# Kernel tuning notes

Measured on AMD Instinct MI355X. Metric: run time of the kernel, lower is better.

Reference implementation:

```python
import jax, jax.numpy as jnp
import numpy as np

N_HEAD = 16

def setup_inputs() -> dict:
    key = jax.random.key(0)
    ks = jax.random.split(key, 8)
    B, S, D = 2, 2048, 1024
    s = 0.02
    return {
        "x": jax.random.normal(ks[0], (B, S, D), dtype=jnp.float32),
        "Wq": jax.random.normal(ks[1], (D, D), dtype=jnp.float32) * s,
        "bq": jax.random.normal(ks[2], (D,), dtype=jnp.float32) * s,
        "Wk": jax.random.normal(ks[3], (D, D), dtype=jnp.float32) * s,
        "Wv": jax.random.normal(ks[4], (D, D), dtype=jnp.float32) * s,
        "bv": jax.random.normal(ks[5], (D,), dtype=jnp.float32) * s,
        "Wo": jax.random.normal(ks[6], (D, D), dtype=jnp.float32) * s,
        "bo": jax.random.normal(ks[7], (D,), dtype=jnp.float32) * s,
    }

def reference(x, Wq, bq, Wk, Wv, bv, Wo, bo):
    B, S, D = x.shape
    H = N_HEAD
    dh = D // H
    scale = dh ** -0.25
    # projections (torch F.linear: x @ W.T + b)
    q = x @ Wq.T + bq
    k = x @ Wk.T              # key has no bias
    v = x @ Wv.T + bv
    # split heads: [B, H, S, dh]
    q = q.reshape(B, S, H, dh).transpose(0, 2, 1, 3) * scale
    k = k.reshape(B, S, H, dh).transpose(0, 2, 1, 3) * scale
    v = v.reshape(B, S, H, dh).transpose(0, 2, 1, 3)
    qk = jnp.einsum('bhqd,bhkd->bhqk', q, k)
    w = jax.nn.softmax(qk.astype(jnp.float32), axis=-1).astype(q.dtype)
    wv = jnp.einsum('bhqk,bhkd->bhqd', w, v)
    wv = wv.transpose(0, 2, 1, 3).reshape(B, S, D)
    out = wv @ Wo.T + bo
    return out, w
```

## Files before the change

### kernel.cpp

```cpp
#include <hip/hip_runtime.h>

typedef float  f32x4 __attribute__((ext_vector_type(4)));
typedef short  s16x8 __attribute__((ext_vector_type(8)));
typedef unsigned short u16x4 __attribute__((ext_vector_type(4)));


static __device__ __forceinline__ unsigned short f2bf(float f) {
  unsigned u = __builtin_bit_cast(unsigned, f);
  u += 0x7fffu + ((u >> 16) & 1u);
  return (unsigned short)(u >> 16);
}

static __device__ __forceinline__ void glds16(const void* g, void* l) {
  __builtin_amdgcn_global_load_lds(
      (const __attribute__((address_space(1))) unsigned int*)g,
      (__attribute__((address_space(3))) unsigned int*)l, 16, 0, 0);
}

__global__ __launch_bounds__(256) void cvt_bf16(const float4* __restrict__ src,
                                                u16x4* __restrict__ dst) {
  int i = blockIdx.x * 256 + threadIdx.x;
  float4 v = src[i];
  u16x4 o = { f2bf(v.x), f2bf(v.y), f2bf(v.z), f2bf(v.w) };
  dst[i] = o;
}

__global__ __launch_bounds__(256) void gemm_nt(const unsigned short* __restrict__ A,
                                               const unsigned short* __restrict__ Bm,
                                               const float* __restrict__ bias,
                                               float scale, int mode,
                                               void* __restrict__ out) {
  __shared__ unsigned short at[128 * 64];
  __shared__ unsigned short bt[128 * 64];
  const int tid = threadIdx.x, lane = tid & 63, wid = tid >> 6;
  const int l15 = lane & 15, l4 = lane >> 4;
  const int nb = (blockIdx.x & 7) * 128, mb = (blockIdx.x >> 3) * 128;
  const int wm = (wid >> 1) * 64, wn = (wid & 1) * 64;

  f32x4 acc[4][4];
#pragma unroll
  for (int mt = 0; mt < 4; ++mt)
#pragma unroll
    for (int nt = 0; nt < 4; ++nt) acc[mt][nt] = {0.f, 0.f, 0.f, 0.f};

  for (int k0 = 0; k0 < 1024; k0 += 64) {
#pragma unroll
    for (int i = 0; i < 4; ++i) {
      int slotbase = (i * 4 + wid) * 64;
      int slot = slotbase + lane;
      int row = slot >> 3;
      int cs = (slot & 7) ^ (row & 7);
      glds16(&A[(mb + row) * 1024 + k0 + cs * 8], &at[slotbase * 8]);
      glds16(&Bm[(nb + row) * 1024 + k0 + cs * 8], &bt[slotbase * 8]);
    }
    __syncthreads();
#pragma unroll
    for (int ks = 0; ks < 2; ++ks) {
      s16x8 af[4], bf[4];
#pragma unroll
      for (int mt = 0; mt < 4; ++mt) {
        int row = wm + mt * 16 + l15;
        af[mt] = *(const s16x8*)((const char*)&at[row * 64] +
                                 ((ks * 64 + l4 * 16) ^ ((row & 7) << 4)));
      }
#pragma unroll
      for (int nt = 0; nt < 4; ++nt) {
        int row = wn + nt * 16 + l15;
        bf[nt] = *(const s16x8*)((const char*)&bt[row * 64] +
                                 ((ks * 64 + l4 * 16) ^ ((row & 7) << 4)));
      }
#pragma unroll
      for (int mt = 0; mt < 4; ++mt)
#pragma unroll
        for (int nt = 0; nt < 4; ++nt)
          acc[mt][nt] = __builtin_amdgcn_mfma_f32_16x16x32_bf16(af[mt], bf[nt],
                                                                acc[mt][nt], 0, 0, 0);
    }
    __syncthreads();
  }

#pragma unroll
  for (int mt = 0; mt < 4; ++mt)
#pragma unroll
    for (int nt = 0; nt < 4; ++nt) {
      int n = nb + wn + nt * 16 + l15;
      float bvv = bias ? bias[n] : 0.0f;
      int m0 = mb + wm + mt * 16 + l4 * 4;
      if (mode == 0) {
#pragma unroll
        for (int r = 0; r < 4; ++r) {
          int m = m0 + r;
          float v = (acc[mt][nt][r] + bvv) * scale;
          int bb = m >> 11, s = m & 2047, hh = n >> 6, d = n & 63;
          ((unsigned short*)out)[(size_t)((bb * 16 + hh) * 2048 + s) * 64 + d] = f2bf(v);
        }
      } else if (mode == 1) {
        int bb = m0 >> 11, s0 = m0 & 2047, hh = n >> 6, d = n & 63;
        u16x4 p;
#pragma unroll
        for (int r = 0; r < 4; ++r) p[r] = f2bf(acc[mt][nt][r] + bvv);
        *(u16x4*)&((unsigned short*)out)[(size_t)((bb * 16 + hh) * 64 + d) * 2048 + s0] = p;
      } else {
#pragma unroll
        for (int r = 0; r < 4; ++r) {
          int m = m0 + r;
          ((float*)out)[(size_t)m * 1024 + n] = acc[mt][nt][r] + bvv;
        }
      }
    }
}

__global__ __launch_bounds__(256) void attn_sumexp(const unsigned short* __restrict__ Q,
                                                   const unsigned short* __restrict__ K,
                                                   float* __restrict__ lsum) {
  __shared__ unsigned short kt[64 * 64];
  const int tid = threadIdx.x, lane = tid & 63, wid = tid >> 6;
  const int l15 = lane & 15, l4 = lane >> 4;
  const int bh = blockIdx.x >> 5;
  const int qb = (blockIdx.x & 31) * 64;
  const int q = qb + wid * 16 + l15;

  s16x8 qf[2];
  qf[0] = *(const s16x8*)&Q[(bh * 2048 + q) * 64 + l4 * 8];
  qf[1] = *(const s16x8*)&Q[(bh * 2048 + q) * 64 + 32 + l4 * 8];

  float acc = 0.f;
  for (int k0 = 0; k0 < 2048; k0 += 64) {
#pragma unroll
    for (int i = 0; i < 2; ++i) {
      int slotbase = (i * 4 + wid) * 64;
      int slot = slotbase + lane;
      int row = slot >> 3;
      int cs = (slot & 7) ^ (row & 7);
      glds16(&K[(bh * 2048 + k0 + row) * 64 + cs * 8], &kt[slotbase * 8]);
    }
    __syncthreads();
#pragma unroll
    for (int ks = 0; ks < 4; ++ks) {
      f32x4 c = {0.f, 0.f, 0.f, 0.f};
      int row = ks * 16 + l15;
#pragma unroll
      for (int t = 0; t < 2; ++t) {
        s16x8 a = *(const s16x8*)((const char*)&kt[row * 64] +
                                  ((t * 64 + l4 * 16) ^ ((row & 7) << 4)));
        c = __builtin_amdgcn_mfma_f32_16x16x32_bf16(a, qf[t], c, 0, 0, 0);
      }
      acc += __expf(c[0]) + __expf(c[1]) + __expf(c[2]) + __expf(c[3]);
    }
    __syncthreads();
  }
  acc += __shfl_xor(acc, 16);
  acc += __shfl_xor(acc, 32);
  if (l4 == 0) lsum[bh * 2048 + q] = acc;
}

__global__ __launch_bounds__(256) void attn_wv(const unsigned short* __restrict__ Q,
                                               const unsigned short* __restrict__ K,
                                               const unsigned short* __restrict__ Vt,
                                               const float* __restrict__ lsum,
                                               float* __restrict__ wout,
                                               unsigned short* __restrict__ wv) {
  __shared__ unsigned short kt[64 * 64];
  __shared__ unsigned short vt[64 * 64];
  __shared__ unsigned short pt[4][16 * 64];
  const int tid = threadIdx.x, lane = tid & 63, wid = tid >> 6;
  const int l15 = lane & 15, l4 = lane >> 4;
  const int bh = blockIdx.x >> 5;
  const int qb = (blockIdx.x & 31) * 64;
  const int q = qb + wid * 16 + l15;

  s16x8 qf[2];
  qf[0] = *(const s16x8*)&Q[(bh * 2048 + q) * 64 + l4 * 8];
  qf[1] = *(const s16x8*)&Q[(bh * 2048 + q) * 64 + 32 + l4 * 8];
  float rcpl = 1.0f / lsum[bh * 2048 + q];
  float* wrow = &wout[((size_t)bh * 2048 + q) * 2048];

  f32x4 oacc[4];
#pragma unroll
  for (int dt = 0; dt < 4; ++dt) oacc[dt] = {0.f, 0.f, 0.f, 0.f};

  for (int k0i = 0; k0i < 32; ++k0i) {
    int k0 = k0i * 64;
#pragma unroll
    for (int i = 0; i < 2; ++i) {
      int slotbase = (i * 4 + wid) * 64;
      int slot = slotbase + lane;
      int row = slot >> 3;
      int cs = (slot & 7) ^ (row & 7);
      glds16(&K[(bh * 2048 + k0 + row) * 64 + cs * 8], &kt[slotbase * 8]);
      glds16(&Vt[(size_t)(bh * 64 + row) * 2048 + k0 + cs * 8], &vt[slotbase * 8]);
    }
    __syncthreads();
#pragma unroll
    for (int ks = 0; ks < 4; ++ks) {
      f32x4 c = {0.f, 0.f, 0.f, 0.f};
      int row = ks * 16 + l15;
#pragma unroll
      for (int t = 0; t < 2; ++t) {
        s16x8 a = *(const s16x8*)((const char*)&kt[row * 64] +
                                  ((t * 64 + l4 * 16) ^ ((row & 7) << 4)));
        c = __builtin_amdgcn_mfma_f32_16x16x32_bf16(a, qf[t], c, 0, 0, 0);
      }
      float w0 = __expf(c[0]) * rcpl, w1 = __expf(c[1]) * rcpl;
      float w2 = __expf(c[2]) * rcpl, w3 = __expf(c[3]) * rcpl;
      f32x4 w4 = {w0, w1, w2, w3};
      *(f32x4*)&wrow[k0 + ks * 16 + l4 * 4] = w4;
      u16x4 pb = {f2bf(w0), f2bf(w1), f2bf(w2), f2bf(w3)};
      *(u16x4*)((char*)&pt[wid][l15 * 64] +
                ((ks * 32 + l4 * 8) ^ ((l15 & 7) << 4))) = pb;
    }
#pragma unroll
    for (int t = 0; t < 2; ++t) {
      s16x8 pa = *(const s16x8*)((const char*)&pt[wid][l15 * 64] +
                                 ((t * 64 + l4 * 16) ^ ((l15 & 7) << 4)));
#pragma unroll
      for (int dt = 0; dt < 4; ++dt) {
        int row = dt * 16 + l15;
        s16x8 vb = *(const s16x8*)((const char*)&vt[row * 64] +
                                   ((t * 64 + l4 * 16) ^ ((row & 7) << 4)));
        oacc[dt] = __builtin_amdgcn_mfma_f32_16x16x32_bf16(pa, vb, oacc[dt], 0, 0, 0);
      }
    }
    __syncthreads();
  }
  int b = bh >> 4, h = bh & 15;
#pragma unroll
  for (int dt = 0; dt < 4; ++dt)
#pragma unroll
    for (int r = 0; r < 4; ++r) {
      int sq = qb + wid * 16 + l4 * 4 + r;
      int d = dt * 16 + l15;
      wv[(size_t)(b * 2048 + sq) * 1024 + h * 64 + d] = f2bf(oacc[dt][r]);
    }
}

extern "C" void kernel_launch(void* const* d_in, const int* in_sizes, int n_in,
                              void* d_out, int out_size, void* d_ws, size_t ws_size,
                              hipStream_t stream) {
  const float* x  = (const float*)d_in[0];
  const float* Wq = (const float*)d_in[1];
  const float* bq = (const float*)d_in[2];
  const float* Wk = (const float*)d_in[3];
  const float* Wv = (const float*)d_in[4];
  const float* bv = (const float*)d_in[5];
  const float* bo = (const float*)d_in[7];
  const float* Wo = (const float*)d_in[6];
  float* out  = (float*)d_out;
  float* wout = out + 4194304;

  unsigned short* xb  = (unsigned short*)d_ws;
  unsigned short* Wqb = xb + 4194304;
  unsigned short* Wkb = Wqb + 1048576;
  unsigned short* Wvb = Wkb + 1048576;
  unsigned short* Wob = Wvb + 1048576;
  unsigned short* Qb  = Wob + 1048576;
  unsigned short* Kb  = Qb + 4194304;
  unsigned short* Vtb = Kb + 4194304;
  float* lsum = (float*)(Vtb + 4194304);
  unsigned short* wvb = xb;

  cvt_bf16<<<4096, 256, 0, stream>>>((const float4*)x,  (u16x4*)xb);
  cvt_bf16<<<1024, 256, 0, stream>>>((const float4*)Wq, (u16x4*)Wqb);
  cvt_bf16<<<1024, 256, 0, stream>>>((const float4*)Wk, (u16x4*)Wkb);
  cvt_bf16<<<1024, 256, 0, stream>>>((const float4*)Wv, (u16x4*)Wvb);
  cvt_bf16<<<1024, 256, 0, stream>>>((const float4*)Wo, (u16x4*)Wob);

  const float kscale = 0.35355339059327373f;
  gemm_nt<<<256, 256, 0, stream>>>(xb, Wqb, bq, kscale, 0, Qb);
  gemm_nt<<<256, 256, 0, stream>>>(xb, Wkb, nullptr, kscale, 0, Kb);
  gemm_nt<<<256, 256, 0, stream>>>(xb, Wvb, bv, 1.0f, 1, Vtb);

  attn_sumexp<<<1024, 256, 0, stream>>>(Qb, Kb, lsum);
  attn_wv<<<1024, 256, 0, stream>>>(Qb, Kb, Vtb, lsum, wout, wvb);

  gemm_nt<<<256, 256, 0, stream>>>(wvb, Wob, bo, 1.0f, 2, out);
}
```

Baseline: 811.1 us.

## Fuse launches, double-buffer attention K/V tiles, and widen per-wave query tiles

Merges the five bf16 conversions into one launch and the three QKV GEMMs into one 768-block launch, with XCD-aware block swizzling. Both attention kernels now double-buffer K (and V) tiles in LDS, prefetching the next tile ahead of compute with explicit vmcnt waits. Each wave now handles 32 queries instead of 16, so every loaded K/V fragment is reused twice. The large softmax-weight output is written with nontemporal stores to avoid polluting the cache. In exchange, LDS use and register pressure per block go up and the grid has half as many blocks, which could lower occupancy.

New measurement: 760.0 us. -6.3%, faster.

```diff
diff --git a/kernel.cpp b/kernel.cpp
--- a/kernel.cpp
+++ b/kernel.cpp
@@ -17,24 +17,49 @@
       (__attribute__((address_space(3))) unsigned int*)l, 16, 0, 0);
 }
 
-__global__ __launch_bounds__(256) void cvt_bf16(const float4* __restrict__ src,
-                                                u16x4* __restrict__ dst) {
-  int i = blockIdx.x * 256 + threadIdx.x;
-  float4 v = src[i];
-  u16x4 o = { f2bf(v.x), f2bf(v.y), f2bf(v.z), f2bf(v.w) };
-  dst[i] = o;
-}
-
-__global__ __launch_bounds__(256) void gemm_nt(const unsigned short* __restrict__ A,
-                                               const unsigned short* __restrict__ Bm,
-                                               const float* __restrict__ bias,
-                                               float scale, int mode,
-                                               void* __restrict__ out) {
-  __shared__ unsigned short at[128 * 64];
-  __shared__ unsigned short bt[128 * 64];
+static __device__ __forceinline__ void ntst4(float* p, f32x4 v) {
+  __builtin_nontemporal_store(v, (f32x4*)p);
+}
+
+static __device__ __forceinline__ void stage64(const unsigned short* gsrc, int gstride,
+                                               unsigned short* lbase, int wid, int lane) {
+#pragma unroll
+  for (int i = 0; i < 2; ++i) {
+    int slotbase = (i * 4 + wid) * 64;
+    int slot = slotbase + lane;
+    int row = slot >> 3;
+    int cs = (slot & 7) ^ (row & 7);
+    glds16(&gsrc[(size_t)row * gstride + cs * 8], &lbase[slotbase * 8]);
+  }
+}
+
+__global__ __launch_bounds__(256) void cvt_all(
+    const float4* __restrict__ x,  const float4* __restrict__ wq,
+    const float4* __restrict__ wk, const float4* __restrict__ wv,
+    const float4* __restrict__ wo,
+    u16x4* __restrict__ xb,  u16x4* __restrict__ wqb,
+    u16x4* __restrict__ wkb, u16x4* __restrict__ wvb,
+    u16x4* __restrict__ wob) {
+  int b = blockIdx.x;
+  const float4* s; u16x4* d; int o;
+  if (b < 4096)      { s = x;  d = xb;  o = b; }
+  else if (b < 5120) { s = wq; d = wqb; o = b - 4096; }
+  else if (b < 6144) { s = wk; d = wkb; o = b - 5120; }
+  else if (b < 7168) { s = wv; d = wvb; o = b - 6144; }
+  else               { s = wo; d = wob; o = b - 7168; }
+  int i = o * 256 + threadIdx.x;
+  float4 v = s[i];
+  u16x4 r = { f2bf(v.x), f2bf(v.y), f2bf(v.z), f2bf(v.w) };
+  d[i] = r;
+}
+
+static __device__ __forceinline__ void gemm_body(
+    int bid, unsigned short* at, unsigned short* bt,
+    const unsigned short* __restrict__ A, const unsigned short* __restrict__ Bm,
+    const float* __restrict__ bias, float scale, int mode, void* __restrict__ out) {
   const int tid = threadIdx.x, lane = tid & 63, wid = tid >> 6;
   const int l15 = lane & 15, l4 = lane >> 4;
-  const int nb = (blockIdx.x & 7) * 128, mb = (blockIdx.x >> 3) * 128;
+  const int nb = (bid & 7) * 128, mb = (bid >> 3) * 128;
   const int wm = (wid >> 1) * 64, wn = (wid & 1) * 64;
 
   f32x4 acc[4][4];
@@ -110,48 +135,86 @@
     }
 }
 
+__global__ __launch_bounds__(256) void gemm_qkv(
+    const unsigned short* __restrict__ xb,
+    const unsigned short* __restrict__ Wqb, const unsigned short* __restrict__ Wkb,
+    const unsigned short* __restrict__ Wvb,
+    const float* __restrict__ bq, const float* __restrict__ bv,
+    unsigned short* __restrict__ Qb, unsigned short* __restrict__ Kb,
+    unsigned short* __restrict__ Vtb, float kscale) {
+  __shared__ unsigned short at[128 * 64];
+  __shared__ unsigned short bt[128 * 64];
+  int sw = (blockIdx.x & 7) * 96 + (blockIdx.x >> 3);
+  int op = sw >> 8, bid = sw & 255;
+  if (op == 0)      gemm_body(bid, at, bt, xb, Wqb, bq,      kscale, 0, Qb);
+  else if (op == 1) gemm_body(bid, at, bt, xb, Wkb, nullptr, kscale, 0, Kb);
+  else              gemm_body(bid, at, bt, xb, Wvb, bv,      1.0f,   1, Vtb);
+}
+
+__global__ __launch_bounds__(256) void gemm_o(
+    const unsigned short* __restrict__ A, const unsigned short* __restrict__ Wob,
+    const float* __restrict__ bo, float* __restrict__ out) {
+  __shared__ unsigned short at[128 * 64];
+  __shared__ unsigned short bt[128 * 64];
+  int sw = (blockIdx.x & 7) * 32 + (blockIdx.x >> 3);
+  gemm_body(sw, at, bt, A, Wob, bo, 1.0f, 2, out);
+}
+
 __global__ __launch_bounds__(256) void attn_sumexp(const unsigned short* __restrict__ Q,
                                                    const unsigned short* __restrict__ K,
                                                    float* __restrict__ lsum) {
-  __shared__ unsigned short kt[64 * 64];
+  __shared__ unsigned short kt[2][64 * 64];
   const int tid = threadIdx.x, lane = tid & 63, wid = tid >> 6;
   const int l15 = lane & 15, l4 = lane >> 4;
-  const int bh = blockIdx.x >> 5;
-  const int qb = (blockIdx.x & 31) * 64;
-  const int q = qb + wid * 16 + l15;
-
-  s16x8 qf[2];
-  qf[0] = *(const s16x8*)&Q[(bh * 2048 + q) * 64 + l4 * 8];
-  qf[1] = *(const s16x8*)&Q[(bh * 2048 + q) * 64 + 32 + l4 * 8];
-
-  float acc = 0.f;
-  for (int k0 = 0; k0 < 2048; k0 += 64) {
-#pragma unroll
-    for (int i = 0; i < 2; ++i) {
-      int slotbase = (i * 4 + wid) * 64;
-      int slot = slotbase + lane;
-      int row = slot >> 3;
-      int cs = (slot & 7) ^ (row & 7);
-      glds16(&K[(bh * 2048 + k0 + row) * 64 + cs * 8], &kt[slotbase * 8]);
-    }
-    __syncthreads();
+  const int sw = (blockIdx.x & 7) * 64 + (blockIdx.x >> 3);
+  const int bh = sw >> 4;
+  const int qb = (sw & 15) * 128;
+  const int q0 = qb + wid * 32 + l15;
+
+  s16x8 qf[2][2];
+#pragma unroll
+  for (int qg = 0; qg < 2; ++qg)
+#pragma unroll
+    for (int t = 0; t < 2; ++t)
+      qf[qg][t] = *(const s16x8*)&Q[(size_t)(bh * 2048 + q0 + qg * 16) * 64 + t * 32 + l4 * 8];
+
+  float acc0 = 0.f, acc1 = 0.f;
+  const unsigned short* Kbh = &K[(size_t)bh * 2048 * 64];
+
+  stage64(&Kbh[0], 64, &kt[0][0], wid, lane);
+  int cur = 0;
+  for (int t = 0; t < 32; ++t) {
+    if (t < 31) {
+      stage64(&Kbh[(size_t)(t + 1) * 64 * 64], 64, &kt[cur ^ 1][0], wid, lane);
+      asm volatile("s_waitcnt vmcnt(2)" ::: "memory");
+    } else {
+      asm volatile("s_waitcnt vmcnt(0)" ::: "memory");
+    }
+    __builtin_amdgcn_sched_barrier(0);
+    __builtin_amdgcn_s_barrier();
 #pragma unroll
     for (int ks = 0; ks < 4; ++ks) {
-      f32x4 c = {0.f, 0.f, 0.f, 0.f};
       int row = ks * 16 + l15;
-#pragma unroll
-      for (int t = 0; t < 2; ++t) {
-        s16x8 a = *(const s16x8*)((const char*)&kt[row * 64] +
-                                  ((t * 64 + l4 * 16) ^ ((row & 7) << 4)));
-        c = __builtin_amdgcn_mfma_f32_16x16x32_bf16(a, qf[t], c, 0, 0, 0);
-      }
-      acc += __expf(c[0]) + __expf(c[1]) + __expf(c[2]) + __expf(c[3]);
-    }
-    __syncthreads();
-  }
-  acc += __shfl_xor(acc, 16);
-  acc += __shfl_xor(acc, 32);
-  if (l4 == 0) lsum[bh * 2048 + q] = acc;
+      const char* rbase = (const char*)&kt[cur][row * 64];
+      s16x8 a0 = *(const s16x8*)(rbase + ((l4 * 16) ^ ((row & 7) << 4)));
+      s16x8 a1 = *(const s16x8*)(rbase + ((64 + l4 * 16) ^ ((row & 7) << 4)));
+      f32x4 c0 = {0.f, 0.f, 0.f, 0.f}, c1 = {0.f, 0.f, 0.f, 0.f};
+      c0 = __builtin_amdgcn_mfma_f32_16x16x32_bf16(a0, qf[0][0], c0, 0, 0, 0);
+      c0 = __builtin_amdgcn_mfma_f32_16x16x32_bf16(a1, qf[0][1], c0, 0, 0, 0);
+      c1 = __builtin_amdgcn_mfma_f32_16x16x32_bf16(a0, qf[1][0], c1, 0, 0, 0);
+      c1 = __builtin_amdgcn_mfma_f32_16x16x32_bf16(a1, qf[1][1], c1, 0, 0, 0);
+      acc0 += __expf(c0[0]) + __expf(c0[1]) + __expf(c0[2]) + __expf(c0[3]);
+      acc1 += __expf(c1[0]) + __expf(c1[1]) + __expf(c1[2]) + __expf(c1[3]);
+    }
+    __builtin_amdgcn_s_barrier();
+    cur ^= 1;
+  }
+  acc0 += __shfl_xor(acc0, 16); acc0 += __shfl_xor(acc0, 32);
+  acc1 += __shfl_xor(acc1, 16); acc1 += __shfl_xor(acc1, 32);
+  if (l4 == 0) {
+    lsum[bh * 2048 + q0] = acc0;
+    lsum[bh * 2048 + q0 + 16] = acc1;
+  }
 }
 
 __global__ __launch_bounds__(256) void attn_wv(const unsigned short* __restrict__ Q,
@@ -160,78 +223,102 @@
                                                const float* __restrict__ lsum,
                                                float* __restrict__ wout,
                                                unsigned short* __restrict__ wv) {
-  __shared__ unsigned short kt[64 * 64];
-  __shared__ unsigned short vt[64 * 64];
-  __shared__ unsigned short pt[4][16 * 64];
+  __shared__ unsigned short kt[2][64 * 64];
+  __shared__ unsigned short vt[2][64 * 64];
+  __shared__ unsigned short pt[4][2][16 * 64];
   const int tid = threadIdx.x, lane = tid & 63, wid = tid >> 6;
   const int l15 = lane & 15, l4 = lane >> 4;
-  const int bh = blockIdx.x >> 5;
-  const int qb = (blockIdx.x & 31) * 64;
-  const int q = qb + wid * 16 + l15;
-
-  s16x8 qf[2];
-  qf[0] = *(const s16x8*)&Q[(bh * 2048 + q) * 64 + l4 * 8];
-  qf[1] = *(const s16x8*)&Q[(bh * 2048 + q) * 64 + 32 + l4 * 8];
-  float rcpl = 1.0f / lsum[bh * 2048 + q];
-  float* wrow = &wout[((size_t)bh * 2048 + q) * 2048];
-
-  f32x4 oacc[4];
-#pragma unroll
-  for (int dt = 0; dt < 4; ++dt) oacc[dt] = {0.f, 0.f, 0.f, 0.f};
-
-  for (int k0i = 0; k0i < 32; ++k0i) {
-    int k0 = k0i * 64;
-#pragma unroll
-    for (int i = 0; i < 2; ++i) {
-      int slotbase = (i * 4 + wid) * 64;
-      int slot = slotbase + lane;
-      int row = slot >> 3;
-      int cs = (slot & 7) ^ (row & 7);
-      glds16(&K[(bh * 2048 + k0 + row) * 64 + cs * 8], &kt[slotbase * 8]);
-      glds16(&Vt[(size_t)(bh * 64 + row) * 2048 + k0 + cs * 8], &vt[slotbase * 8]);
-    }
-    __syncthreads();
+  const int sw = (blockIdx.x & 7) * 64 + (blockIdx.x >> 3);
+  const int bh = sw >> 4;
+  const int qb = (sw & 15) * 128;
+  const int q0 = qb + wid * 32 + l15;
+
+  s16x8 qf[2][2];
+#pragma unroll
+  for (int qg = 0; qg < 2; ++qg)
+#pragma unroll
+    for (int t = 0; t < 2; ++t)
+      qf[qg][t] = *(const s16x8*)&Q[(size_t)(bh * 2048 + q0 + qg * 16) * 64 + t * 32 + l4 * 8];
+  float rcpl0 = 1.0f / lsum[bh * 2048 + q0];
+  float rcpl1 = 1.0f / lsum[bh * 2048 + q0 + 16];
+  float* wrow0 = &wout[((size_t)bh * 2048 + q0) * 2048];
+  float* wrow1 = wrow0 + (size_t)16 * 2048;
+
+  f32x4 oacc[2][4];
+#pragma unroll
+  for (int qg = 0; qg < 2; ++qg)
+#pragma unroll
+    for (int dt = 0; dt < 4; ++dt) oacc[qg][dt] = {0.f, 0.f, 0.f, 0.f};
+
+  const unsigned short* Kbh = &K[(size_t)bh * 2048 * 64];
+  const unsigned short* Vbh = &Vt[(size_t)bh * 64 * 2048];
+
+  stage64(&Kbh[0], 64, &kt[0][0], wid, lane);
+  stage64(&Vbh[0], 2048, &vt[0][0], wid, lane);
+  int cur = 0;
+  for (int t = 0; t < 32; ++t) {
+    int k0 = t * 64;
+    if (t < 31) {
+      stage64(&Kbh[(size_t)(t + 1) * 64 * 64], 64, &kt[cur ^ 1][0], wid, lane);
+      stage64(&Vbh[k0 + 64], 2048, &vt[cur ^ 1][0], wid, lane);
+      asm volatile("s_waitcnt vmcnt(4)" ::: "memory");
+    } else {
+      asm volatile("s_waitcnt vmcnt(0)" ::: "memory");
+    }
+    __builtin_amdgcn_sched_barrier(0);
+    __builtin_amdgcn_s_barrier();
+
 #pragma unroll
     for (int ks = 0; ks < 4; ++ks) {
-      f32x4 c = {0.f, 0.f, 0.f, 0.f};
       int row = ks * 16 + l15;
-#pragma unroll
-      for (int t = 0; t < 2; ++t) {
-        s16x8 a = *(const s16x8*)((const char*)&kt[row * 64] +
-                                  ((t * 64 + l4 * 16) ^ ((row & 7) << 4)));
-        c = __builtin_amdgcn_mfma_f32_16x16x32_bf16(a, qf[t], c, 0, 0, 0);
-      }
-      float w0 = __expf(c[0]) * rcpl, w1 = __expf(c[1]) * rcpl;
-      float w2 = __expf(c[2]) * rcpl, w3 = __expf(c[3]) * rcpl;
-      f32x4 w4 = {w0, w1, w2, w3};
-      *(f32x4*)&wrow[k0 + ks * 16 + l4 * 4] = w4;
-      u16x4 pb = {f2bf(w0), f2bf(w1), f2bf(w2), f2bf(w3)};
-      *(u16x4*)((char*)&pt[wid][l15 * 64] +
-                ((ks * 32 + l4 * 8) ^ ((l15 & 7) << 4))) = pb;
-    }
-#pragma unroll
-    for (int t = 0; t < 2; ++t) {
-      s16x8 pa = *(const s16x8*)((const char*)&pt[wid][l15 * 64] +
-                                 ((t * 64 + l4 * 16) ^ ((l15 & 7) << 4)));
+      const char* rbase = (const char*)&kt[cur][row * 64];
+      s16x8 a0 = *(const s16x8*)(rbase + ((l4 * 16) ^ ((row & 7) << 4)));
+      s16x8 a1 = *(const s16x8*)(rbase + ((64 + l4 * 16) ^ ((row & 7) << 4)));
+      f32x4 c0 = {0.f, 0.f, 0.f, 0.f}, c1 = {0.f, 0.f, 0.f, 0.f};
+      c0 = __builtin_amdgcn_mfma_f32_16x16x32_bf16(a0, qf[0][0], c0, 0, 0, 0);
+      c0 = __builtin_amdgcn_mfma_f32_16x16x32_bf16(a1, qf[0][1], c0, 0, 0, 0);
+      c1 = __builtin_amdgcn_mfma_f32_16x16x32_bf16(a0, qf[1][0], c1, 0, 0, 0);
+      c1 = __builtin_amdgcn_mfma_f32_16x16x32_bf16(a1, qf[1][1], c1, 0, 0, 0);
+      float w00 = __expf(c0[0]) * rcpl0, w01 = __expf(c0[1]) * rcpl0;
+      float w02 = __expf(c0[2]) * rcpl0, w03 = __expf(c0[3]) * rcpl0;
+      float w10 = __expf(c1[0]) * rcpl1, w11 = __expf(c1[1]) * rcpl1;
+      float w12 = __expf(c1[2]) * rcpl1, w13 = __expf(c1[3]) * rcpl1;
+      ntst4(&wrow0[k0 + ks * 16 + l4 * 4], (f32x4){w00, w01, w02, w03});
+      ntst4(&wrow1[k0 + ks * 16 + l4 * 4], (f32x4){w10, w11, w12, w13});
+      u16x4 pb0 = {f2bf(w00), f2bf(w01), f2bf(w02), f2bf(w03)};
+      u16x4 pb1 = {f2bf(w10), f2bf(w11), f2bf(w12), f2bf(w13)};
+      *(u16x4*)((char*)&pt[wid][0][l15 * 64] + ((ks * 32 + l4 * 8) ^ ((l15 & 7) << 4))) = pb0;
+      *(u16x4*)((char*)&pt[wid][1][l15 * 64] + ((ks * 32 + l4 * 8) ^ ((l15 & 7) << 4))) = pb1;
+    }
+#pragma unroll
+    for (int t2 = 0; t2 < 2; ++t2) {
+      s16x8 pa0 = *(const s16x8*)((char*)&pt[wid][0][l15 * 64] +
+                                  ((t2 * 64 + l4 * 16) ^ ((l15 & 7) << 4)));
+      s16x8 pa1 = *(const s16x8*)((char*)&pt[wid][1][l15 * 64] +
+                                  ((t2 * 64 + l4 * 16) ^ ((l15 & 7) << 4)));
 #pragma unroll
       for (int dt = 0; dt < 4; ++dt) {
-        int row = dt * 16 + l15;
-        s16x8 vb = *(const s16x8*)((const char*)&vt[row * 64] +
-                                   ((t * 64 + l4 * 16) ^ ((row & 7) << 4)));
-        oacc[dt] = __builtin_amdgcn_mfma_f32_16x16x32_bf16(pa, vb, oacc[dt], 0, 0, 0);
-      }
-    }
-    __syncthreads();
+        int vrow = dt * 16 + l15;
+        s16x8 vb = *(const s16x8*)((const char*)&vt[cur][vrow * 64] +
+                                   ((t2 * 64 + l4 * 16) ^ ((vrow & 7) << 4)));
+        oacc[0][dt] = __builtin_amdgcn_mfma_f32_16x16x32_bf16(pa0, vb, oacc[0][dt], 0, 0, 0);
+        oacc[1][dt] = __builtin_amdgcn_mfma_f32_16x16x32_bf16(pa1, vb, oacc[1][dt], 0, 0, 0);
+      }
+    }
+    __builtin_amdgcn_s_barrier();
+    cur ^= 1;
   }
   int b = bh >> 4, h = bh & 15;
 #pragma unroll
-  for (int dt = 0; dt < 4; ++dt)
-#pragma unroll
-    for (int r = 0; r < 4; ++r) {
-      int sq = qb + wid * 16 + l4 * 4 + r;
-      int d = dt * 16 + l15;
-      wv[(size_t)(b * 2048 + sq) * 1024 + h * 64 + d] = f2bf(oacc[dt][r]);
-    }
+  for (int qg = 0; qg < 2; ++qg)
+#pragma unroll
+    for (int dt = 0; dt < 4; ++dt)
+#pragma unroll
+      for (int r = 0; r < 4; ++r) {
+        int sq = qb + wid * 32 + qg * 16 + l4 * 4 + r;
+        int d = dt * 16 + l15;
+        wv[(size_t)(b * 2048 + sq) * 1024 + h * 64 + d] = f2bf(oacc[qg][dt][r]);
+      }
 }
 
 extern "C" void kernel_launch(void* const* d_in, const int* in_sizes, int n_in,
@@ -243,8 +330,8 @@
   const float* Wk = (const float*)d_in[3];
   const float* Wv = (const float*)d_in[4];
   const float* bv = (const float*)d_in[5];
+  const float* Wo = (const float*)d_in[6];
   const float* bo = (const float*)d_in[7];
-  const float* Wo = (const float*)d_in[6];
   float* out  = (float*)d_out;
   float* wout = out + 4194304;
 
@@ -259,19 +346,17 @@
   float* lsum = (float*)(Vtb + 4194304);
   unsigned short* wvb = xb;
 
-  cvt_bf16<<<4096, 256, 0, stream>>>((const float4*)x,  (u16x4*)xb);
-  cvt_bf16<<<1024, 256, 0, stream>>>((const float4*)Wq, (u16x4*)Wqb);
-  cvt_bf16<<<1024, 256, 0, stream>>>((const float4*)Wk, (u16x4*)Wkb);
-  cvt_bf16<<<1024, 256, 0, stream>>>((const float4*)Wv, (u16x4*)Wvb);
-  cvt_bf16<<<1024, 256, 0, stream>>>((const float4*)Wo, (u16x4*)Wob);
+  cvt_all<<<8192, 256, 0, stream>>>((const float4*)x, (const float4*)Wq,
+                                    (const float4*)Wk, (const float4*)Wv,
+                                    (const float4*)Wo,
+                                    (u16x4*)xb, (u16x4*)Wqb, (u16x4*)Wkb,
+                                    (u16x4*)Wvb, (u16x4*)Wob);
 
   const float kscale = 0.35355339059327373f;
-  gemm_nt<<<256, 256, 0, stream>>>(xb, Wqb, bq, kscale, 0, Qb);
-  gemm_nt<<<256, 256, 0, stream>>>(xb, Wkb, nullptr, kscale, 0, Kb);
-  gemm_nt<<<256, 256, 0, stream>>>(xb, Wvb, bv, 1.0f, 1, Vtb);
-
-  attn_sumexp<<<1024, 256, 0, stream>>>(Qb, Kb, lsum);
-  attn_wv<<<1024, 256, 0, stream>>>(Qb, Kb, Vtb, lsum, wout, wvb);
-
-  gemm_nt<<<256, 256, 0, stream>>>(wvb, Wob, bo, 1.0f, 2, out);
-}
+  gemm_qkv<<<768, 256, 0, stream>>>(xb, Wqb, Wkb, Wvb, bq, bv, Qb, Kb, Vtb, kscale);
+
+  attn_sumexp<<<512, 256, 0, stream>>>(Qb, Kb, lsum);
+  attn_wv<<<512, 256, 0, stream>>>(Qb, Kb, Vtb, lsum, wout, wvb);
+
+  gemm_o<<<256, 256, 0, stream>>>(wvb, Wob, bo, out);
+}
```
